# Kernel tuning notes

Measured on AMD Instinct MI355X. Metric: run time of the kernel, lower is better.

The kernel has to match this reference:

```python
import jax, jax.numpy as jnp
import numpy as np


def setup_inputs() -> dict:
    key = jax.random.key(0)
    ks = jax.random.split(key, 7)
    B, T, U = 8, 200, 50
    D_enc, D_dec, J, V = 512, 512, 512, 1024
    s = 0.05
    return {
        "h_enc": jax.random.normal(ks[0], (B, T, 1, D_enc), dtype=jnp.float32),
        "h_dec": jax.random.normal(ks[1], (B, 1, U, D_dec), dtype=jnp.float32),
        "W_enc": jax.random.normal(ks[2], (J, D_enc), dtype=jnp.float32) * s,
        "b_enc": jax.random.normal(ks[3], (J,), dtype=jnp.float32) * s,
        "W_dec": jax.random.normal(ks[4], (J, D_dec), dtype=jnp.float32) * s,
        "W_out": jax.random.normal(ks[5], (V, J), dtype=jnp.float32) * s,
        "b_out": jax.random.normal(ks[6], (V,), dtype=jnp.float32) * s,
    }


def reference(h_enc, h_dec, W_enc, b_enc, W_dec, W_out, b_out):
    # lin_enc: (B,T,1,D_enc) -> (B,T,1,J) ; lin_dec (no bias): (B,1,U,D_dec) -> (B,1,U,J)
    e = jnp.einsum("btod,jd->btoj", h_enc, W_enc) + b_enc
    d = jnp.einsum("boud,jd->bouj", h_dec, W_dec)
    # broadcast add -> (B,T,U,J), Tanh activation
    z = jnp.tanh(e + d)
    # lin_out: (B,T,U,J) -> (B,T,U,V)
    return jnp.einsum("btuj,vj->btuv", z, W_out) + b_out
```

## Files before the change

kernel.cpp:

```cpp
#include <hip/hip_runtime.h>
#include <hip/hip_bf16.h>


typedef short bf16x8 __attribute__((ext_vector_type(8)));
typedef float fx4 __attribute__((ext_vector_type(4)));

static constexpr int KD = 512;
static constexpr int V = 1024;

__device__ inline unsigned short f2bf(float f) {
    union { float f; unsigned u; } v; v.f = f;
    unsigned r = v.u + 0x7fffu + ((v.u >> 16) & 1u);
    return (unsigned short)(r >> 16);
}
__device__ inline float bf2f(unsigned short h) {
    union { float f; unsigned u; } v; v.u = ((unsigned)h) << 16; return v.f;
}
__device__ inline float fast_tanh(float x) {
    float p = __builtin_amdgcn_exp2f(x * 2.885390081777926f);
    return 1.0f - 2.0f * __builtin_amdgcn_rcpf(p + 1.0f);
}
__device__ inline void gld_lds16(const void* g, void* l) {
    __builtin_amdgcn_global_load_lds(
        (const __attribute__((address_space(1))) void*)g,
        (__attribute__((address_space(3))) void*)l, 16, 0, 0);
}

__global__ __launch_bounds__(256) void prep(
    const float* __restrict__ h_enc, const float* __restrict__ W_enc,
    const float* __restrict__ b_enc, const float* __restrict__ h_dec,
    const float* __restrict__ W_dec, const float* __restrict__ W_out,
    float* __restrict__ e, float* __restrict__ dd, unsigned short* __restrict__ Wb) {
    const int bx = blockIdx.x;
    const int t = threadIdx.x;
    if (bx >= 256) {
        int i = ((bx - 256) * 256 + t) * 8;
        fx4 a = *(const fx4*)(W_out + i);
        fx4 b = *(const fx4*)(W_out + i + 4);
        unsigned short p[8];
        #pragma unroll
        for (int j = 0; j < 4; j++) { p[j] = f2bf(a[j]); p[j + 4] = f2bf(b[j]); }
        *(bf16x8*)(Wb + i) = *(bf16x8*)p;
        return;
    }
    const float* A; const float* W; const float* bias; float* out;
    int Mrows, mb, nb;
    if (bx < 200) { A = h_enc; W = W_enc; bias = b_enc; out = e;  Mrows = 1600; mb = bx >> 3; nb = bx & 7; }
    else { int b2 = bx - 200; A = h_dec; W = W_dec; bias = nullptr; out = dd; Mrows = 400; mb = b2 >> 3; nb = b2 & 7; }

    __shared__ unsigned short As[64 * 32];
    __shared__ unsigned short Ws[64 * 32];
    const int lane = t & 63, wid = t >> 6;
    const int m0 = mb * 64, n0 = nb * 64;
    const int wm = (wid & 1) * 32, wn = (wid >> 1) * 32;

    fx4 acc[2][2];
    const fx4 z4 = {0.f, 0.f, 0.f, 0.f};
    acc[0][0] = z4; acc[0][1] = z4; acc[1][0] = z4; acc[1][1] = z4;

    const int sr = t >> 2;
    const int skc = (t & 3) * 8;
    const int ar = (m0 + sr < Mrows) ? (m0 + sr) : (Mrows - 1);
    const float* Ap = A + (size_t)ar * KD + skc;
    const float* Wp = W + (size_t)(n0 + sr) * KD + skc;
    unsigned short* asl = &As[sr * 32 + skc];
    unsigned short* wsl = &Ws[sr * 32 + skc];

    for (int ph = 0; ph < 2; ph++) {
        const int wmode = (ph == 1);
        for (int kb = 0; kb < 16; kb++) {
            const int k0 = kb * 32;
            fx4 a0 = *(const fx4*)(Ap + k0);
            fx4 a1 = *(const fx4*)(Ap + k0 + 4);
            fx4 w0 = *(const fx4*)(Wp + k0);
            fx4 w1 = *(const fx4*)(Wp + k0 + 4);
            unsigned short pa[8], pw[8];
            #pragma unroll
            for (int i = 0; i < 4; i++) {
                unsigned short h;
                pa[i] = f2bf(a0[i]); pa[i + 4] = f2bf(a1[i]);
                h = f2bf(w0[i]); pw[i]     = wmode ? f2bf(w0[i] - bf2f(h)) : h;
                h = f2bf(w1[i]); pw[i + 4] = wmode ? f2bf(w1[i] - bf2f(h)) : h;
            }
            *(bf16x8*)asl = *(bf16x8*)pa;
            *(bf16x8*)wsl = *(bf16x8*)pw;
            __syncthreads();
            bf16x8 af[2], wf[2];
            #pragma unroll
            for (int f = 0; f < 2; f++) {
                af[f] = *(const bf16x8*)&As[(wm + f * 16 + (lane & 15)) * 32 + (lane >> 4) * 8];
                wf[f] = *(const bf16x8*)&Ws[(wn + f * 16 + (lane & 15)) * 32 + (lane >> 4) * 8];
            }
            #pragma unroll
            for (int fm = 0; fm < 2; fm++)
                #pragma unroll
                for (int fn = 0; fn < 2; fn++)
                    acc[fm][fn] = __builtin_amdgcn_mfma_f32_16x16x32_bf16(
                        af[fm], wf[fn], acc[fm][fn], 0, 0, 0);
            __syncthreads();
        }
    }
    const int colb = n0 + wn + (lane & 15);
    const int rowb = m0 + wm + (lane >> 4) * 4;
    float bo[2];
    bo[0] = bias ? bias[colb] : 0.f;
    bo[1] = bias ? bias[colb + 16] : 0.f;
    #pragma unroll
    for (int fm = 0; fm < 2; fm++) {
        #pragma unroll
        for (int r = 0; r < 4; r++) {
            int row = rowb + fm * 16 + r;
            if (row < Mrows) {
                float* op = out + (size_t)row * KD;
                op[colb] = acc[fm][0][r] + bo[0];
                op[colb + 16] = acc[fm][1][r] + bo[1];
            }
        }
    }
}

__global__ __launch_bounds__(256) void tanh_z(
    const float* __restrict__ e, const float* __restrict__ d,
    unsigned short* __restrict__ Z) {
    const int t = threadIdx.x;
    const int m = blockIdx.x * 4 + (t >> 6);
    const int kc = (t & 63) * 8;
    const int bt = m / 50;
    const int u = m - bt * 50;
    const int b = m / 10000;
    const float* ep = e + (size_t)bt * KD + kc;
    const float* dp = d + (size_t)(b * 50 + u) * KD + kc;
    fx4 e0 = *(const fx4*)ep, e1 = *(const fx4*)(ep + 4);
    fx4 d0 = *(const fx4*)dp, d1 = *(const fx4*)(dp + 4);
    unsigned short p[8];
    #pragma unroll
    for (int i = 0; i < 4; i++) {
        p[i] = f2bf(fast_tanh(e0[i] + d0[i]));
        p[i + 4] = f2bf(fast_tanh(e1[i] + d1[i]));
    }
    *(bf16x8*)(Z + (size_t)m * KD + kc) = *(bf16x8*)p;
}

__global__ __launch_bounds__(256) void gemm_out_k(
    const unsigned short* __restrict__ Z, const unsigned short* __restrict__ Wb,
    const float* __restrict__ b_out, float* __restrict__ out) {
    __shared__ unsigned short As[2][128 * 32];
    __shared__ unsigned short Bs[2][128 * 32];
    const int t = threadIdx.x;
    const int lane = t & 63, wid = t >> 6;
    const int bid = blockIdx.x;
    const int n0 = (bid & 7) * 128;
    const int m0 = (bid >> 3) * 128;
    const int wm = (wid & 1) * 64, wn = (wid >> 1) * 64;

    fx4 acc[4][4];
    const fx4 z4 = {0.f, 0.f, 0.f, 0.f};
    #pragma unroll
    for (int i = 0; i < 4; i++)
        #pragma unroll
        for (int j = 0; j < 4; j++) acc[i][j] = z4;

    size_t gA[2], gB[2];
    int lofs[2];
    #pragma unroll
    for (int q = 0; q < 2; q++) {
        int c = (wid * 2 + q) * 64 + lane;
        int r = c >> 2, kc = (c & 3) * 8;
        gA[q] = (size_t)(m0 + r) * KD + kc;
        gB[q] = (size_t)(n0 + r) * KD + kc;
        lofs[q] = (wid * 2 + q) * 512;
    }

    for (int kb = 0; kb < 8; kb++) {
        const int k0 = kb * 64;
        #pragma unroll
        for (int h = 0; h < 2; h++)
            #pragma unroll
            for (int q = 0; q < 2; q++) {
                gld_lds16(Z + gA[q] + k0 + h * 32, &As[h][lofs[q]]);
                gld_lds16(Wb + gB[q] + k0 + h * 32, &Bs[h][lofs[q]]);
            }
        __syncthreads();
        #pragma unroll
        for (int h = 0; h < 2; h++) {
            bf16x8 af[4], bf[4];
            #pragma unroll
            for (int f = 0; f < 4; f++) {
                af[f] = *(const bf16x8*)&As[h][(wm + f * 16 + (lane & 15)) * 32 + (lane >> 4) * 8];
                bf[f] = *(const bf16x8*)&Bs[h][(wn + f * 16 + (lane & 15)) * 32 + (lane >> 4) * 8];
            }
            #pragma unroll
            for (int fm = 0; fm < 4; fm++)
                #pragma unroll
                for (int fn = 0; fn < 4; fn++)
                    acc[fm][fn] = __builtin_amdgcn_mfma_f32_16x16x32_bf16(
                        af[fm], bf[fn], acc[fm][fn], 0, 0, 0);
        }
        __syncthreads();
    }

    const int colb = n0 + wn + (lane & 15);
    const int rowb = m0 + wm + (lane >> 4) * 4;
    float bo[4];
    #pragma unroll
    for (int fn = 0; fn < 4; fn++) bo[fn] = b_out[colb + fn * 16];
    #pragma unroll
    for (int fm = 0; fm < 4; fm++) {
        #pragma unroll
        for (int r = 0; r < 4; r++) {
            float* op = out + (size_t)(rowb + fm * 16 + r) * V;
            #pragma unroll
            for (int fn = 0; fn < 4; fn++)
                op[colb + fn * 16] = acc[fm][fn][r] + bo[fn];
        }
    }
}

extern "C" void kernel_launch(void* const* d_in, const int* in_sizes, int n_in,
                              void* d_out, int out_size, void* d_ws, size_t ws_size,
                              hipStream_t stream) {
    const float* h_enc = (const float*)d_in[0];
    const float* h_dec = (const float*)d_in[1];
    const float* W_enc = (const float*)d_in[2];
    const float* b_enc = (const float*)d_in[3];
    const float* W_dec = (const float*)d_in[4];
    const float* W_out = (const float*)d_in[5];
    const float* b_out = (const float*)d_in[6];
    float* out = (float*)d_out;

    float* e = (float*)d_ws;
    float* dd = e + 1600 * KD;
    unsigned short* Wb = (unsigned short*)(dd + 400 * KD);
    unsigned short* Zb = Wb + (size_t)V * KD;

    prep<<<512, 256, 0, stream>>>(h_enc, W_enc, b_enc, h_dec, W_dec, W_out, e, dd, Wb);
    tanh_z<<<20000, 256, 0, stream>>>(e, dd, Zb);
    gemm_out_k<<<5000, 256, 0, stream>>>(Zb, Wb, b_out, out);
}
```

Before: 474.2 us.

## Use 256x256 tiles with 8-wave ping-pong pipelined MFMA GEMM

Replaces the 128x128-tile output GEMM with a 256x256-tile, 512-thread kernel. It double-buffers LDS and interleaves global-to-LDS prefetch of the next K slice with MFMA phases, using explicit waitcnt, barriers and setprio. The larger tiles raise arithmetic intensity and cut redundant loads of Z and W. The costs are larger LDS use (128KB per block), a padded last M tile that needs row guards, and fewer blocks for load balancing.

```diff
diff --git a/kernel.cpp b/kernel.cpp
--- a/kernel.cpp
+++ b/kernel.cpp
@@ -141,62 +141,138 @@
     *(bf16x8*)(Z + (size_t)m * KD + kc) = *(bf16x8*)p;
 }
 
-__global__ __launch_bounds__(256) void gemm_out_k(
+__global__ __launch_bounds__(512, 2) void gemm_out_k8(
     const unsigned short* __restrict__ Z, const unsigned short* __restrict__ Wb,
     const float* __restrict__ b_out, float* __restrict__ out) {
-    __shared__ unsigned short As[2][128 * 32];
-    __shared__ unsigned short Bs[2][128 * 32];
+    __shared__ unsigned short As[2][2][256 * 32];
+    __shared__ unsigned short Bs[2][2][256 * 32];
     const int t = threadIdx.x;
     const int lane = t & 63, wid = t >> 6;
     const int bid = blockIdx.x;
-    const int n0 = (bid & 7) * 128;
-    const int m0 = (bid >> 3) * 128;
-    const int wm = (wid & 1) * 64, wn = (wid >> 1) * 64;
-
-    fx4 acc[4][4];
+    const int n0 = (bid & 3) * 256;
+    const int m0 = (bid >> 2) * 256;
+    const int wm = (wid >> 2) * 128;
+    const int wn = (wid & 3) * 64;
+
+    fx4 acc[8][4];
     const fx4 z4 = {0.f, 0.f, 0.f, 0.f};
     #pragma unroll
-    for (int i = 0; i < 4; i++)
+    for (int i = 0; i < 8; i++)
         #pragma unroll
         for (int j = 0; j < 4; j++) acc[i][j] = z4;
 
     size_t gA[2], gB[2];
-    int lofs[2];
+    int lb[2];
     #pragma unroll
     for (int q = 0; q < 2; q++) {
-        int c = (wid * 2 + q) * 64 + lane;
-        int r = c >> 2, kc = (c & 3) * 8;
-        gA[q] = (size_t)(m0 + r) * KD + kc;
-        gB[q] = (size_t)(n0 + r) * KD + kc;
-        lofs[q] = (wid * 2 + q) * 512;
-    }
-
-    for (int kb = 0; kb < 8; kb++) {
-        const int k0 = kb * 64;
-        #pragma unroll
-        for (int h = 0; h < 2; h++)
-            #pragma unroll
-            for (int q = 0; q < 2; q++) {
-                gld_lds16(Z + gA[q] + k0 + h * 32, &As[h][lofs[q]]);
-                gld_lds16(Wb + gB[q] + k0 + h * 32, &Bs[h][lofs[q]]);
-            }
-        __syncthreads();
-        #pragma unroll
-        for (int h = 0; h < 2; h++) {
-            bf16x8 af[4], bf[4];
-            #pragma unroll
-            for (int f = 0; f < 4; f++) {
-                af[f] = *(const bf16x8*)&As[h][(wm + f * 16 + (lane & 15)) * 32 + (lane >> 4) * 8];
-                bf[f] = *(const bf16x8*)&Bs[h][(wn + f * 16 + (lane & 15)) * 32 + (lane >> 4) * 8];
-            }
-            #pragma unroll
-            for (int fm = 0; fm < 4; fm++)
-                #pragma unroll
-                for (int fn = 0; fn < 4; fn++)
-                    acc[fm][fn] = __builtin_amdgcn_mfma_f32_16x16x32_bf16(
-                        af[fm], bf[fn], acc[fm][fn], 0, 0, 0);
-        }
-        __syncthreads();
+        int rl = (wid * 2 + q) * 16 + (lane >> 2);
+        int kc = (lane & 3) * 8;
+        int ra = m0 + rl; if (ra > 79999) ra = 79999;
+        gA[q] = (size_t)ra * KD + kc;
+        gB[q] = (size_t)(n0 + rl) * KD + kc;
+        lb[q] = (wid * 2 + q) * 512;
+    }
+
+    const int offA = (wm + (lane & 15)) * 32 + (lane >> 4) * 8;
+    const int offB = (wn + (lane & 15)) * 32 + (lane >> 4) * 8;
+
+    gld_lds16(Z + gA[0], &As[0][0][lb[0]]);
+    gld_lds16(Z + gA[1], &As[0][0][lb[1]]);
+    gld_lds16(Wb + gB[0], &Bs[0][0][lb[0]]);
+    gld_lds16(Wb + gB[1], &Bs[0][0][lb[1]]);
+    gld_lds16(Z + gA[0] + 32, &As[0][1][lb[0]]);
+    gld_lds16(Z + gA[1] + 32, &As[0][1][lb[1]]);
+    gld_lds16(Wb + gB[0] + 32, &Bs[0][1][lb[0]]);
+    gld_lds16(Wb + gB[1] + 32, &Bs[0][1][lb[1]]);
+    asm volatile("s_waitcnt vmcnt(4)" ::: "memory");
+    __builtin_amdgcn_s_barrier();
+
+    #pragma unroll 2
+    for (int kt = 0; kt < 8; kt++) {
+        const int cb = kt & 1, cb2 = cb ^ 1;
+        const size_t ko = (size_t)(kt + 1) * 64;
+        const bool pf = (kt < 7);
+        bf16x8 afA[4], afB[4], bfA[4];
+
+        #pragma unroll
+        for (int i = 0; i < 4; i++) afA[i] = *(const bf16x8*)&As[cb][0][offA + i * 512];
+        #pragma unroll
+        for (int i = 0; i < 4; i++) bfA[i] = *(const bf16x8*)&Bs[cb][0][offB + i * 512];
+        if (pf) {
+            gld_lds16(Z + gA[0] + ko, &As[cb2][0][lb[0]]);
+            gld_lds16(Z + gA[1] + ko, &As[cb2][0][lb[1]]);
+        }
+        __builtin_amdgcn_s_barrier();
+        asm volatile("s_waitcnt lgkmcnt(0)" ::: "memory");
+        __builtin_amdgcn_sched_barrier(0);
+        __builtin_amdgcn_s_setprio(1);
+        #pragma unroll
+        for (int m = 0; m < 4; m++)
+            #pragma unroll
+            for (int n = 0; n < 4; n++)
+                acc[m][n] = __builtin_amdgcn_mfma_f32_16x16x32_bf16(afA[m], bfA[n], acc[m][n], 0, 0, 0);
+        __builtin_amdgcn_s_setprio(0);
+        __builtin_amdgcn_s_barrier();
+
+        #pragma unroll
+        for (int i = 0; i < 4; i++) afB[i] = *(const bf16x8*)&As[cb][0][offA + (4 + i) * 512];
+        if (pf) {
+            gld_lds16(Wb + gB[0] + ko, &Bs[cb2][0][lb[0]]);
+            gld_lds16(Wb + gB[1] + ko, &Bs[cb2][0][lb[1]]);
+            asm volatile("s_waitcnt vmcnt(4)" ::: "memory");
+        } else {
+            asm volatile("s_waitcnt vmcnt(0)" ::: "memory");
+        }
+        __builtin_amdgcn_s_barrier();
+        asm volatile("s_waitcnt lgkmcnt(0)" ::: "memory");
+        __builtin_amdgcn_sched_barrier(0);
+        __builtin_amdgcn_s_setprio(1);
+        #pragma unroll
+        for (int m = 0; m < 4; m++)
+            #pragma unroll
+            for (int n = 0; n < 4; n++)
+                acc[4 + m][n] = __builtin_amdgcn_mfma_f32_16x16x32_bf16(afB[m], bfA[n], acc[4 + m][n], 0, 0, 0);
+        __builtin_amdgcn_s_setprio(0);
+        __builtin_amdgcn_s_barrier();
+
+        #pragma unroll
+        for (int i = 0; i < 4; i++) afA[i] = *(const bf16x8*)&As[cb][1][offA + i * 512];
+        #pragma unroll
+        for (int i = 0; i < 4; i++) bfA[i] = *(const bf16x8*)&Bs[cb][1][offB + i * 512];
+        if (pf) {
+            gld_lds16(Z + gA[0] + ko + 32, &As[cb2][1][lb[0]]);
+            gld_lds16(Z + gA[1] + ko + 32, &As[cb2][1][lb[1]]);
+        }
+        __builtin_amdgcn_s_barrier();
+        asm volatile("s_waitcnt lgkmcnt(0)" ::: "memory");
+        __builtin_amdgcn_sched_barrier(0);
+        __builtin_amdgcn_s_setprio(1);
+        #pragma unroll
+        for (int m = 0; m < 4; m++)
+            #pragma unroll
+            for (int n = 0; n < 4; n++)
+                acc[m][n] = __builtin_amdgcn_mfma_f32_16x16x32_bf16(afA[m], bfA[n], acc[m][n], 0, 0, 0);
+        __builtin_amdgcn_s_setprio(0);
+        __builtin_amdgcn_s_barrier();
+
+        #pragma unroll
+        for (int i = 0; i < 4; i++) afB[i] = *(const bf16x8*)&As[cb][1][offA + (4 + i) * 512];
+        if (pf) {
+            gld_lds16(Wb + gB[0] + ko + 32, &Bs[cb2][1][lb[0]]);
+            gld_lds16(Wb + gB[1] + ko + 32, &Bs[cb2][1][lb[1]]);
+            asm volatile("s_waitcnt vmcnt(4)" ::: "memory");
+        }
+        __builtin_amdgcn_s_barrier();
+        asm volatile("s_waitcnt lgkmcnt(0)" ::: "memory");
+        __builtin_amdgcn_sched_barrier(0);
+        __builtin_amdgcn_s_setprio(1);
+        #pragma unroll
+        for (int m = 0; m < 4; m++)
+            #pragma unroll
+            for (int n = 0; n < 4; n++)
+                acc[4 + m][n] = __builtin_amdgcn_mfma_f32_16x16x32_bf16(afB[m], bfA[n], acc[4 + m][n], 0, 0, 0);
+        __builtin_amdgcn_s_setprio(0);
+        __builtin_amdgcn_s_barrier();
     }
 
     const int colb = n0 + wn + (lane & 15);
@@ -205,13 +281,16 @@
     #pragma unroll
     for (int fn = 0; fn < 4; fn++) bo[fn] = b_out[colb + fn * 16];
     #pragma unroll
-    for (int fm = 0; fm < 4; fm++) {
+    for (int fm = 0; fm < 8; fm++) {
         #pragma unroll
         for (int r = 0; r < 4; r++) {
-            float* op = out + (size_t)(rowb + fm * 16 + r) * V;
-            #pragma unroll
-            for (int fn = 0; fn < 4; fn++)
-                op[colb + fn * 16] = acc[fm][fn][r] + bo[fn];
+            const int row = rowb + fm * 16 + r;
+            if (row < 80000) {
+                float* op = out + (size_t)row * V;
+                #pragma unroll
+                for (int fn = 0; fn < 4; fn++)
+                    op[colb + fn * 16] = acc[fm][fn][r] + bo[fn];
+            }
         }
     }
 }
@@ -235,5 +314,5 @@
 
     prep<<<512, 256, 0, stream>>>(h_enc, W_enc, b_enc, h_dec, W_dec, W_out, e, dd, Wb);
     tanh_z<<<20000, 256, 0, stream>>>(e, dd, Zb);
-    gemm_out_k<<<5000, 256, 0, stream>>>(Zb, Wb, b_out, out);
-}
+    gemm_out_k8<<<313 * 4, 512, 0, stream>>>(Zb, Wb, b_out, out);
+}
```

Result: faster. 455.0 us (-4.0%).

## Rewrite output GEMM with 256x256 tiles, 4-stage LDS pipeline and swizzled LDS

Applied to the files above, without the earlier changes.

The output GEMM now uses 512-thread blocks computing 256x256 tiles with a 4-deep LDS ring buffer. Global-to-LDS loads are issued three stages ahead and synchronised with explicit vmcnt waits and a single barrier per k-step. The LDS layout is XOR-swizzled to reduce bank conflicts, and MFMA bursts are wrapped in setprio. The goal is to hide memory latency and improve reuse. The cost is higher register pressure (32 accumulators per thread) and ragged row handling for the last tile.

```diff
diff --git a/kernel.cpp b/kernel.cpp
--- a/kernel.cpp
+++ b/kernel.cpp
@@ -141,62 +141,92 @@
     *(bf16x8*)(Z + (size_t)m * KD + kc) = *(bf16x8*)p;
 }
 
-__global__ __launch_bounds__(256) void gemm_out_k(
+__global__ __launch_bounds__(512, 2) void gemm_out_r(
     const unsigned short* __restrict__ Z, const unsigned short* __restrict__ Wb,
     const float* __restrict__ b_out, float* __restrict__ out) {
-    __shared__ unsigned short As[2][128 * 32];
-    __shared__ unsigned short Bs[2][128 * 32];
+    __shared__ unsigned short As[4][256 * 32];
+    __shared__ unsigned short Bs[4][256 * 32];
     const int t = threadIdx.x;
     const int lane = t & 63, wid = t >> 6;
     const int bid = blockIdx.x;
-    const int n0 = (bid & 7) * 128;
-    const int m0 = (bid >> 3) * 128;
-    const int wm = (wid & 1) * 64, wn = (wid >> 1) * 64;
-
-    fx4 acc[4][4];
+    const int n0 = (bid & 3) * 256;
+    const int m0 = (bid >> 2) * 256;
+    const int wm = (wid >> 2) * 128;
+    const int wn = (wid & 3) * 64;
+
+    fx4 acc[8][4];
     const fx4 z4 = {0.f, 0.f, 0.f, 0.f};
     #pragma unroll
-    for (int i = 0; i < 4; i++)
+    for (int i = 0; i < 8; i++)
         #pragma unroll
         for (int j = 0; j < 4; j++) acc[i][j] = z4;
 
     size_t gA[2], gB[2];
-    int lofs[2];
-    #pragma unroll
-    for (int q = 0; q < 2; q++) {
-        int c = (wid * 2 + q) * 64 + lane;
-        int r = c >> 2, kc = (c & 3) * 8;
-        gA[q] = (size_t)(m0 + r) * KD + kc;
-        gB[q] = (size_t)(n0 + r) * KD + kc;
-        lofs[q] = (wid * 2 + q) * 512;
-    }
-
-    for (int kb = 0; kb < 8; kb++) {
-        const int k0 = kb * 64;
-        #pragma unroll
-        for (int h = 0; h < 2; h++)
-            #pragma unroll
-            for (int q = 0; q < 2; q++) {
-                gld_lds16(Z + gA[q] + k0 + h * 32, &As[h][lofs[q]]);
-                gld_lds16(Wb + gB[q] + k0 + h * 32, &Bs[h][lofs[q]]);
-            }
-        __syncthreads();
-        #pragma unroll
-        for (int h = 0; h < 2; h++) {
-            bf16x8 af[4], bf[4];
-            #pragma unroll
-            for (int f = 0; f < 4; f++) {
-                af[f] = *(const bf16x8*)&As[h][(wm + f * 16 + (lane & 15)) * 32 + (lane >> 4) * 8];
-                bf[f] = *(const bf16x8*)&Bs[h][(wn + f * 16 + (lane & 15)) * 32 + (lane >> 4) * 8];
-            }
-            #pragma unroll
-            for (int fm = 0; fm < 4; fm++)
-                #pragma unroll
-                for (int fn = 0; fn < 4; fn++)
-                    acc[fm][fn] = __builtin_amdgcn_mfma_f32_16x16x32_bf16(
-                        af[fm], bf[fn], acc[fm][fn], 0, 0, 0);
-        }
-        __syncthreads();
+    int lb[2];
+    {
+        const int kcs = ((lane & 3) ^ ((lane >> 3) & 3)) * 8;
+        #pragma unroll
+        for (int q = 0; q < 2; q++) {
+            int rl = q * 128 + wid * 16 + (lane >> 2);
+            int ra = m0 + rl; if (ra > 79999) ra = 79999;
+            gA[q] = (size_t)ra * KD + kcs;
+            gB[q] = (size_t)(n0 + rl) * KD + kcs;
+            lb[q] = q * 4096 + wid * 512;
+        }
+    }
+
+    const int xsl = ((lane >> 4) ^ (((lane & 15) >> 1) & 3)) * 8;
+    const int offA = (wm + (lane & 15)) * 32 + xsl;
+    const int offB = (wn + (lane & 15)) * 32 + xsl;
+
+    #pragma unroll
+    for (int p = 0; p < 3; p++) {
+        const size_t ko = (size_t)p * 32;
+        gld_lds16(Z + gA[0] + ko, &As[p][lb[0]]);
+        gld_lds16(Z + gA[1] + ko, &As[p][lb[1]]);
+        gld_lds16(Wb + gB[0] + ko, &Bs[p][lb[0]]);
+        gld_lds16(Wb + gB[1] + ko, &Bs[p][lb[1]]);
+    }
+    asm volatile("s_waitcnt vmcnt(8)" ::: "memory");
+    __builtin_amdgcn_s_barrier();
+
+    #pragma unroll 4
+    for (int kt = 0; kt < 16; kt++) {
+        const int r = kt & 3;
+        const int s = (kt + 3) & 3;
+        const size_t ko = (size_t)(kt + 3) * 32;
+
+        if (kt <= 12) {
+            gld_lds16(Z + gA[0] + ko, &As[s][lb[0]]);
+            gld_lds16(Z + gA[1] + ko, &As[s][lb[1]]);
+            gld_lds16(Wb + gB[0] + ko, &Bs[s][lb[0]]);
+            gld_lds16(Wb + gB[1] + ko, &Bs[s][lb[1]]);
+        }
+
+        bf16x8 af[8], bf[4];
+        #pragma unroll
+        for (int f = 0; f < 8; f++) af[f] = *(const bf16x8*)&As[r][offA + f * 512];
+        #pragma unroll
+        for (int f = 0; f < 4; f++) bf[f] = *(const bf16x8*)&Bs[r][offB + f * 512];
+
+        asm volatile("s_waitcnt lgkmcnt(0)" ::: "memory");
+        __builtin_amdgcn_sched_barrier(0);
+        __builtin_amdgcn_s_setprio(1);
+        #pragma unroll
+        for (int m = 0; m < 8; m++)
+            #pragma unroll
+            for (int n = 0; n < 4; n++)
+                acc[m][n] = __builtin_amdgcn_mfma_f32_16x16x32_bf16(af[m], bf[n], acc[m][n], 0, 0, 0);
+        __builtin_amdgcn_s_setprio(0);
+
+        if (kt <= 12) {
+            asm volatile("s_waitcnt vmcnt(8)" ::: "memory");
+        } else if (kt == 13) {
+            asm volatile("s_waitcnt vmcnt(4)" ::: "memory");
+        } else if (kt == 14) {
+            asm volatile("s_waitcnt vmcnt(0)" ::: "memory");
+        }
+        __builtin_amdgcn_s_barrier();
     }
 
     const int colb = n0 + wn + (lane & 15);
@@ -205,13 +235,16 @@
     #pragma unroll
     for (int fn = 0; fn < 4; fn++) bo[fn] = b_out[colb + fn * 16];
     #pragma unroll
-    for (int fm = 0; fm < 4; fm++) {
+    for (int fm = 0; fm < 8; fm++) {
         #pragma unroll
         for (int r = 0; r < 4; r++) {
-            float* op = out + (size_t)(rowb + fm * 16 + r) * V;
-            #pragma unroll
-            for (int fn = 0; fn < 4; fn++)
-                op[colb + fn * 16] = acc[fm][fn][r] + bo[fn];
+            const int row = rowb + fm * 16 + r;
+            if (row < 80000) {
+                float* op = out + (size_t)row * V;
+                #pragma unroll
+                for (int fn = 0; fn < 4; fn++)
+                    op[colb + fn * 16] = acc[fm][fn][r] + bo[fn];
+            }
         }
     }
 }
@@ -235,5 +268,5 @@
 
     prep<<<512, 256, 0, stream>>>(h_enc, W_enc, b_enc, h_dec, W_dec, W_out, e, dd, Wb);
     tanh_z<<<20000, 256, 0, stream>>>(e, dd, Zb);
-    gemm_out_k<<<5000, 256, 0, stream>>>(Zb, Wb, b_out, out);
-}
+    gemm_out_r<<<313 * 4, 512, 0, stream>>>(Zb, Wb, b_out, out);
+}
```

New measurement: 453.0 us. 1.05x faster.
